# Kernel tuning notes

Hardware: AMD Instinct MI355X
Metric: run time of the kernel (lower is better)

## Reference

```python
import jax, jax.numpy as jnp
import numpy as np
from jax import lax

B, L = 128, 256
DW, DC = 100, 30
H = 400          # hidden_size (bidirectional total)
HD = H // 2      # per-direction hidden
NT = 18          # tag vocab size (BIOES)
VW, VC = 400000, 50000


def setup_inputs():
    key = jax.random.key(0)
    ks = iter(jax.random.split(key, 64))
    rn = lambda shape, s=0.1: jax.random.normal(next(ks), shape, jnp.float32) * s
    inp = {
        "words": jax.random.randint(next(ks), (B, L), 0, VW),
        "cap_words": jax.random.randint(next(ks), (B, L), 0, VC),
        "seq_len": jax.random.randint(next(ks), (B,), L // 2, L + 1),
        "target": jax.random.randint(next(ks), (B, L), 0, NT),
        "word_emb": rn((VW, DW)),
        "char_emb": rn((VC, DC)),
    }
    for l, din in ((0, DW + DC), (1, H)):
        for d in ("f", "b"):
            inp[f"W_ih_l{l}{d}"] = rn((4 * HD, din))
            inp[f"W_hh_l{l}{d}"] = rn((4 * HD, HD))
            inp[f"b_ih_l{l}{d}"] = rn((4 * HD,))
            inp[f"b_hh_l{l}{d}"] = rn((4 * HD,))
    inp["Wf"], inp["bf"] = rn((NT, HD)), jnp.zeros((NT,), jnp.float32)
    inp["Wb"], inp["bb"] = rn((NT, HD)), jnp.zeros((NT,), jnp.float32)
    inp["trans"] = rn((NT, NT))
    return inp


def _lstm_dir(x, W_ih, W_hh, b_ih, b_hh):
    # x: [B, L, D] -> hidden states [B, L, HD]; torch gate order i, f, g, o
    Bsz = x.shape[0]
    def step(carry, xt):
        h, c = carry
        g = xt @ W_ih.T + b_ih + h @ W_hh.T + b_hh
        i, f, gg, o = jnp.split(g, 4, axis=-1)
        c = jax.nn.sigmoid(f) * c + jax.nn.sigmoid(i) * jnp.tanh(gg)
        h = jax.nn.sigmoid(o) * jnp.tanh(c)
        return (h, c), h
    init = (jnp.zeros((Bsz, HD), x.dtype), jnp.zeros((Bsz, HD), x.dtype))
    _, hs = lax.scan(step, init, jnp.swapaxes(x, 0, 1))
    return jnp.swapaxes(hs, 0, 1)


def _rev(x, seq_len):
    # reverse each sequence within its true length (padding stays in place),
    # emulating pack_padded_sequence semantics for the backward direction
    t = jnp.arange(x.shape[1])[None, :]
    idx = jnp.where(t < seq_len[:, None], seq_len[:, None] - 1 - t, t)
    return jnp.take_along_axis(x, idx[:, :, None], axis=1)


def _crf_nll(logits, tags, mask, trans):
    # normalizer: forward algorithm, logsumexp scan over time with mask
    def step(alpha, inp):
        emit, m = inp  # emit: [B, NT], m: [B] bool
        new = jax.nn.logsumexp(alpha[:, :, None] + trans[None] + emit[:, None, :], axis=1)
        return jnp.where(m[:, None], new, alpha), None
    emits = jnp.swapaxes(logits, 0, 1)  # [L, B, NT]
    ms = jnp.swapaxes(mask, 0, 1)
    alpha, _ = lax.scan(step, emits[0], (emits[1:], ms[1:]))
    z = jax.nn.logsumexp(alpha, axis=1)
    # gold path score
    mf = mask.astype(logits.dtype)
    emit_sc = jnp.take_along_axis(logits, tags[:, :, None], axis=2)[:, :, 0]
    gold = jnp.sum(emit_sc * mf, axis=1) + jnp.sum(trans[tags[:, :-1], tags[:, 1:]] * mf[:, 1:], axis=1)
    return z - gold  # per-sample negative log-likelihood, shape [B]


def _model(words, cap_words, seq_len, target, word_emb, char_emb,
           W_ih_l0f, W_hh_l0f, b_ih_l0f, b_hh_l0f, W_ih_l0b, W_hh_l0b, b_ih_l0b, b_hh_l0b,
           W_ih_l1f, W_hh_l1f, b_ih_l1f, b_hh_l1f, W_ih_l1b, W_hh_l1b, b_ih_l1b, b_hh_l1b,
           Wf, bf, Wb, bb, trans):
    mask = jnp.arange(L)[None, :] < seq_len[:, None]  # [B, L] bool
    mf = mask.astype(jnp.float32)[:, :, None]
    x = jnp.concatenate([word_emb[words], char_emb[cap_words]], axis=-1)
    layers = (((W_ih_l0f, W_hh_l0f, b_ih_l0f, b_hh_l0f), (W_ih_l0b, W_hh_l0b, b_ih_l0b, b_hh_l0b)),
              ((W_ih_l1f, W_hh_l1f, b_ih_l1f, b_hh_l1f), (W_ih_l1b, W_hh_l1b, b_ih_l1b, b_hh_l1b)))
    h = x
    for fp, bp in layers:
        fwd = _lstm_dir(h, *fp)
        bwd = _rev(_lstm_dir(_rev(h, seq_len), *bp), seq_len)
        h = jnp.concatenate([fwd, bwd], axis=-1) * mf  # zero padded steps like packed LSTM
    forwards, backwards = h[..., :HD], h[..., HD:]
    logits = forwards @ Wf.T + bf + backwards @ Wb.T + bb
    return _crf_nll(logits, target, mask, trans)


def reference(words, cap_words, seq_len, target, word_emb, char_emb,
              W_ih_l0f, W_hh_l0f, b_ih_l0f, b_hh_l0f, W_ih_l0b, W_hh_l0b, b_ih_l0b, b_hh_l0b,
              W_ih_l1f, W_hh_l1f, b_ih_l1f, b_hh_l1f, W_ih_l1b, W_hh_l1b, b_ih_l1b, b_hh_l1b,
              Wf, bf, Wb, bb, trans):
    return _model(words, cap_words, seq_len, target, word_emb, char_emb,
                  W_ih_l0f, W_hh_l0f, b_ih_l0f, b_hh_l0f, W_ih_l0b, W_hh_l0b, b_ih_l0b, b_hh_l0b,
                  W_ih_l1f, W_hh_l1f, b_ih_l1f, b_hh_l1f, W_ih_l1b, W_hh_l1b, b_ih_l1b, b_hh_l1b,
                  Wf, bf, Wb, bb, trans)
```

## Files before the change

### kernel.cpp

```cpp
#include <hip/hip_runtime.h>
#include <math.h>

#define B_   128
#define L_   256
#define DW_  100
#define DC_  30
#define HD_  200
#define NT_  18
#define SG   4
#define KP0  160
#define KP1  416

typedef _Float16 half8 __attribute__((ext_vector_type(8)));
typedef _Float16 half4 __attribute__((ext_vector_type(4)));
typedef float    f32x4 __attribute__((ext_vector_type(4)));

__device__ __forceinline__ float frcp_(float x) { return __builtin_amdgcn_rcpf(x); }
__device__ __forceinline__ float sigm_(float x) { return frcp_(1.0f + __expf(-x)); }
__device__ __forceinline__ float tanh_(float x) { return 1.0f - 2.0f * frcp_(1.0f + __expf(2.0f * x)); }

__device__ __forceinline__ void barrier_lgkm() {
    asm volatile("s_waitcnt lgkmcnt(0)" ::: "memory");
    __builtin_amdgcn_s_barrier();
    asm volatile("" ::: "memory");
}

__global__ void k_embed(const int* __restrict__ words, const int* __restrict__ caps,
                        const float* __restrict__ wemb, const float* __restrict__ cemb,
                        _Float16* __restrict__ x) {
    int pos = blockIdx.x;
    int w = words[pos], c = caps[pos];
    _Float16* xp = x + (size_t)pos * KP0;
    for (int t = threadIdx.x; t < KP0; t += blockDim.x) {
        float v = 0.f;
        if (t < DW_) v = wemb[(size_t)w * DW_ + t];
        else if (t < DW_ + DC_) v = cemb[(size_t)c * DC_ + (t - DW_)];
        xp[t] = (_Float16)v;
    }
}

__global__ void k_perm_ih16(const float* __restrict__ src, _Float16* __restrict__ dst,
                            int K, int Kpad, int colOff) {
    int i = blockIdx.x * blockDim.x + threadIdx.x;
    if (i >= 800 * Kpad) return;
    int r = i / Kpad, k = i - r * Kpad;
    int jh = r % 200, g = r / 200;
    int col = colOff + (jh << 2) + g;
    dst[(size_t)col * Kpad + k] = (k < K) ? (_Float16)src[(size_t)r * K + k] : (_Float16)0.f;
}

__global__ void k_bias_perm(const float* bi_f, const float* bh_f,
                            const float* bi_b, const float* bh_b, float* bias) {
    int j = blockIdx.x * blockDim.x + threadIdx.x;
    if (j >= 1600) return;
    int dir = j / 800, r = j - dir * 800;
    int col = dir * 800 + ((r % 200) << 2) + (r / 200);
    bias[col] = dir ? (bi_b[r] + bh_b[r]) : (bi_f[r] + bh_f[r]);
}

__global__ void k_wlog(const float* __restrict__ Wf, const float* __restrict__ bfv,
                       const float* __restrict__ Wb, const float* __restrict__ bbv,
                       float* __restrict__ wlog, float* __restrict__ blog) {
    int i = blockIdx.x * blockDim.x + threadIdx.x;
    if (i < NT_ * 400) {
        int t = i / 400, k = i - t * 400;
        wlog[i] = (k < HD_) ? Wf[t * HD_ + k] : Wb[t * HD_ + (k - HD_)];
    }
    if (i < NT_) blog[i] = bfv[i] + bbv[i];
}

__global__ __launch_bounds__(256) void k_gemm16(const _Float16* __restrict__ A,
                                                const _Float16* __restrict__ Bt,
                                                const float* __restrict__ bias,
                                                _Float16* __restrict__ C,
                                                int Kpad) {
    __shared__ __align__(16) _Float16 sA[128 * 40];
    __shared__ __align__(16) _Float16 sB[64 * 40];
    const int tid = threadIdx.x;
    const int w = tid >> 6, l = tid & 63, l15 = l & 15, lq = l >> 4;
    const int m0 = blockIdx.y * 128, n0 = blockIdx.x * 64;
    const int rw = (w >> 1) * 64, cw = (w & 1) * 32;
    f32x4 acc[4][2];
    #pragma unroll
    for (int i = 0; i < 4; i++)
        #pragma unroll
        for (int j = 0; j < 2; j++) acc[i][j] = f32x4{0.f, 0.f, 0.f, 0.f};

    for (int k0 = 0; k0 < Kpad; k0 += 32) {
        {
            int m = tid >> 1, c = (tid & 1) << 4;
            const _Float16* ap = A + (size_t)(m0 + m) * Kpad + k0 + c;
            *(half8*)&sA[m * 40 + c]     = *(const half8*)ap;
            *(half8*)&sA[m * 40 + c + 8] = *(const half8*)(ap + 8);
        }
        {
            int n = tid >> 2, k8 = (tid & 3) << 3;
            *(half8*)&sB[n * 40 + k8] = *(const half8*)&Bt[(size_t)(n0 + n) * Kpad + k0 + k8];
        }
        __syncthreads();
        half8 aF[4], bF[2];
        #pragma unroll
        for (int i = 0; i < 4; i++) aF[i] = *(const half8*)&sA[(rw + i * 16 + l15) * 40 + lq * 8];
        #pragma unroll
        for (int j = 0; j < 2; j++) bF[j] = *(const half8*)&sB[(cw + j * 16 + l15) * 40 + lq * 8];
        #pragma unroll
        for (int i = 0; i < 4; i++)
            #pragma unroll
            for (int j = 0; j < 2; j++)
                acc[i][j] = __builtin_amdgcn_mfma_f32_16x16x32_f16(aF[i], bF[j], acc[i][j], 0, 0, 0);
        __syncthreads();
    }
    #pragma unroll
    for (int j = 0; j < 2; j++) {
        int n = n0 + cw + j * 16 + l15;
        float bv = bias[n];
        #pragma unroll
        for (int i = 0; i < 4; i++) {
            int mrow = m0 + rw + i * 16 + lq * 4;
            #pragma unroll
            for (int r = 0; r < 4; r++)
                C[(size_t)(mrow + r) * 1600 + n] = (_Float16)(acc[i][j][r] + bv);
        }
    }
}

__global__ __launch_bounds__(512, 2) void k_scan7(const _Float16* __restrict__ gates,
                                                  const float* __restrict__ Whh_f,
                                                  const float* __restrict__ Whh_b,
                                                  const int* __restrict__ seq_len,
                                                  _Float16* __restrict__ hout, int ldH) {
    const int dir = blockIdx.x & 1;
    const int b0  = (blockIdx.x >> 1) * SG;
    const int tid = threadIdx.x;
    const int w   = tid >> 6;
    const int l   = tid & 63;
    const int l15 = l & 15;
    const int lq  = l >> 4;

    __shared__ __align__(16) _Float16 hA[2][16 * 232];
    __shared__ __align__(16) _Float16 bEx[2 * 7 * 512];
    __shared__ __align__(16) float    gD[8 * 448];
    __shared__ int ssl[SG];

    const float* W = dir ? Whh_b : Whh_f;
    const int nT = (w < 2) ? 7 : 6;
    const int nCell = nT * 16;

    half8 Breg[6][7];
    #pragma unroll
    for (int i = 0; i < 6; i++) {
        int n  = (w * 6 + i) * 16 + l15;
        int jh = n >> 2, g = n & 3;
        const float* Wr = W + (size_t)(g * 200 + jh) * 200;
        #pragma unroll
        for (int kt = 0; kt < 7; kt++) {
            int k0 = kt * 32 + lq * 8;
            half8 f;
            #pragma unroll
            for (int j = 0; j < 8; j++) {
                int k = k0 + j;
                f[j] = (k < 200) ? (_Float16)Wr[k] : (_Float16)0.f;
            }
            Breg[i][kt] = f;
        }
    }
    if (w < 2) {
        int n  = (48 + w) * 16 + l15;
        int jh = n >> 2, g = n & 3;
        const float* Wr = W + (size_t)(g * 200 + jh) * 200;
        for (int kt = 0; kt < 7; kt++) {
            int k0 = kt * 32 + lq * 8;
            half8 f;
            for (int j = 0; j < 8; j++) {
                int k = k0 + j;
                f[j] = (k < 200) ? (_Float16)Wr[k] : (_Float16)0.f;
            }
            *(half8*)&bEx[(w * 7 + kt) * 512 + l * 8] = f;
        }
    }
    for (int i = tid; i < 2 * 16 * 232; i += 512) (&hA[0][0])[i] = (_Float16)0.f;
    if (tid < SG) ssl[tid] = seq_len[b0 + tid];

    const int  v    = tid;
    const bool stv  = v < 400;
    const int  m_st = v / 100;
    const int  u_st = v - m_st * 100;

    const int cA = l;
    const int iA = cA >> 4, qA = (cA >> 2) & 3, mA = cA & 3;
    const int tgA = (iA < 6) ? (w * 6 + iA) : (48 + w);
    const int hcA = tgA * 4 + qA;
    const int cB = l + 64;
    const int iB = cB >> 4, qB = (cB >> 2) & 3, mB = cB & 3;
    const bool vB = cB < nCell;
    const int tgB = (iB < 6) ? (w * 6 + iB) : (48 + w);
    const int hcB = tgB * 4 + qB;
    float csA = 0.f, csB = 0.f;

    __syncthreads();

    const int slA = ssl[mA];
    const int slB = ssl[mB];
    const int slb_st = stv ? ssl[m_st] : 0;
    const _Float16* gA_base = gates + ((size_t)(b0 + mA) * L_) * 1600 + dir * 800 + 4 * hcA;
    const _Float16* gB_base = gates + ((size_t)(b0 + mB) * L_) * 1600 + dir * 800 + 4 * hcB;
    _Float16* hout_base = hout + (size_t)(b0 + m_st) * L_ * ldH + dir * HD_ + 2 * u_st;

    auto rowOf = [&](int t, int sl) -> int {
        return dir ? ((t < sl) ? sl - 1 - t : t) : t;
    };

    half4 gA0, gA1, gB0, gB1;
    gA0 = *(const half4*)(gA_base + (size_t)rowOf(0, slA) * 1600);
    gA1 = *(const half4*)(gA_base + (size_t)rowOf(1, slA) * 1600);
    if (vB) {
        gB0 = *(const half4*)(gB_base + (size_t)rowOf(0, slB) * 1600);
        gB1 = *(const half4*)(gB_base + (size_t)rowOf(1, slB) * 1600);
    }

    const f32x4 Cz = {0.f, 0.f, 0.f, 0.f};
    for (int t = 0; t < L_; t++) {
        const int p = t & 1;

        if (t > 0 && stv) {
            int tp = t - 1;
            int row = dir ? ((tp < slb_st) ? slb_st - 1 - tp : tp) : tp;
            unsigned int val = (tp < slb_st) ? *(const unsigned int*)&hA[p][m_st * 232 + 2 * u_st] : 0u;
            *(unsigned int*)(hout_base + (size_t)row * ldH) = val;
        }

        f32x4 C[7];
        #pragma unroll
        for (int i = 0; i < 7; i++) C[i] = Cz;
        #pragma unroll
        for (int kt = 0; kt < 7; kt++) {
            half8 hF = *(const half8*)&hA[p][l15 * 232 + kt * 32 + lq * 8];
            #pragma unroll
            for (int i = 0; i < 6; i++)
                C[i] = __builtin_amdgcn_mfma_f32_16x16x32_f16(Breg[i][kt], hF, C[i], 0, 0, 0);
            if (w < 2) {
                half8 bF = *(const half8*)&bEx[(w * 7 + kt) * 512 + l * 8];
                C[6] = __builtin_amdgcn_mfma_f32_16x16x32_f16(bF, hF, C[6], 0, 0, 0);
            }
        }

        if (l15 < 4) {
            #pragma unroll
            for (int i = 0; i < 6; i++)
                *(f32x4*)&gD[w * 448 + (i * 16 + lq * 4 + l15) * 4] = C[i];
            if (w < 2)
                *(f32x4*)&gD[w * 448 + (6 * 16 + lq * 4 + l15) * 4] = C[6];
        }

        {
            f32x4 gv = *(const f32x4*)&gD[w * 448 + cA * 4];
            float xi = gv[0] + (float)gA0[0];
            float xf = gv[1] + (float)gA0[1];
            float xg = gv[2] + (float)gA0[2];
            float xo = gv[3] + (float)gA0[3];
            float cn = sigm_(xf) * csA + sigm_(xi) * tanh_(xg);
            csA = cn;
            hA[1 - p][mA * 232 + hcA] = (_Float16)(sigm_(xo) * tanh_(cn));
        }
        if (vB) {
            f32x4 gv = *(const f32x4*)&gD[w * 448 + cB * 4];
            float xi = gv[0] + (float)gB0[0];
            float xf = gv[1] + (float)gB0[1];
            float xg = gv[2] + (float)gB0[2];
            float xo = gv[3] + (float)gB0[3];
            float cn = sigm_(xf) * csB + sigm_(xi) * tanh_(xg);
            csB = cn;
            hA[1 - p][mB * 232 + hcB] = (_Float16)(sigm_(xo) * tanh_(cn));
        }

        gA0 = gA1;
        gB0 = gB1;
        if (t + 2 < L_) {
            gA1 = *(const half4*)(gA_base + (size_t)rowOf(t + 2, slA) * 1600);
            if (vB) gB1 = *(const half4*)(gB_base + (size_t)rowOf(t + 2, slB) * 1600);
        }

        barrier_lgkm();
    }
    if (stv) {
        int tp = L_ - 1;
        int row = dir ? ((tp < slb_st) ? slb_st - 1 - tp : tp) : tp;
        unsigned int val = (tp < slb_st) ? *(const unsigned int*)&hA[0][m_st * 232 + 2 * u_st] : 0u;
        *(unsigned int*)(hout_base + (size_t)row * ldH) = val;
    }
}

__global__ __launch_bounds__(256) void k_logits(const _Float16* __restrict__ h1,
                                                const float* __restrict__ wlog,
                                                const float* __restrict__ blog,
                                                float* __restrict__ logits) {
    __shared__ float sh[8][400];
    __shared__ float sw[NT_ * 400];
    int p0 = blockIdx.x * 8;
    for (int i = threadIdx.x; i < 8 * 400; i += 256)
        sh[i / 400][i % 400] = (float)h1[(size_t)p0 * 400 + i];
    for (int i = threadIdx.x; i < NT_ * 400; i += 256) sw[i] = wlog[i];
    __syncthreads();
    if (threadIdx.x < 8 * NT_) {
        int pi = threadIdx.x / NT_, tg = threadIdx.x % NT_;
        float a = blog[tg];
        #pragma unroll 4
        for (int k = 0; k < 400; k++) a += sh[pi][k] * sw[tg * 400 + k];
        logits[((size_t)(p0 + pi)) * NT_ + tg] = a;
    }
}

__global__ __launch_bounds__(64) void k_crf(const float* __restrict__ logits,
                                            const int* __restrict__ target,
                                            const int* __restrict__ seq_len,
                                            const float* __restrict__ trans,
                                            float* __restrict__ out) {
    int b = blockIdx.x, tid = threadIdx.x;
    __shared__ float str[NT_ * NT_];
    __shared__ float alpha[NT_];
    __shared__ float sgold[1];
    for (int i = tid; i < NT_ * NT_; i += 64) str[i] = trans[i];
    int sl = seq_len[b];
    const float* lg = logits + (size_t)b * L_ * NT_;
    const int* tg = target + (size_t)b * L_;
    if (tid < NT_) alpha[tid] = lg[tid];
    float gacc = 0.f;
    for (int t = tid; t < L_; t += 64) {
        if (t < sl) {
            gacc += lg[t * NT_ + tg[t]];
            if (t >= 1) gacc += trans[tg[t - 1] * NT_ + tg[t]];
        }
    }
    #pragma unroll
    for (int off = 32; off; off >>= 1) gacc += __shfl_down(gacc, off);
    if (tid == 0) sgold[0] = gacc;
    __syncthreads();
    for (int t = 1; t < L_; t++) {
        if (t < sl) {
            float vv = 0.f;
            if (tid < NT_) {
                float mx = -1e30f;
                #pragma unroll
                for (int i = 0; i < NT_; i++) mx = fmaxf(mx, alpha[i] + str[i * NT_ + tid]);
                float s = 0.f;
                #pragma unroll
                for (int i = 0; i < NT_; i++) s += __expf(alpha[i] + str[i * NT_ + tid] - mx);
                vv = mx + __logf(s) + lg[t * NT_ + tid];
            }
            __syncthreads();
            if (tid < NT_) alpha[tid] = vv;
            __syncthreads();
        }
    }
    if (tid == 0) {
        float mx = -1e30f;
        for (int i = 0; i < NT_; i++) mx = fmaxf(mx, alpha[i]);
        float s = 0.f;
        for (int i = 0; i < NT_; i++) s += __expf(alpha[i] - mx);
        out[b] = (mx + __logf(s)) - sgold[0];
    }
}

extern "C" void kernel_launch(void* const* d_in, const int* in_sizes, int n_in,
                              void* d_out, int out_size, void* d_ws, size_t ws_size,
                              hipStream_t stream) {
    const int*   words  = (const int*)d_in[0];
    const int*   caps   = (const int*)d_in[1];
    const int*   seq    = (const int*)d_in[2];
    const int*   target = (const int*)d_in[3];
    const float* wemb   = (const float*)d_in[4];
    const float* cemb   = (const float*)d_in[5];
    const float* Wih0f  = (const float*)d_in[6];
    const float* Whh0f  = (const float*)d_in[7];
    const float* bih0f  = (const float*)d_in[8];
    const float* bhh0f  = (const float*)d_in[9];
    const float* Wih0b  = (const float*)d_in[10];
    const float* Whh0b  = (const float*)d_in[11];
    const float* bih0b  = (const float*)d_in[12];
    const float* bhh0b  = (const float*)d_in[13];
    const float* Wih1f  = (const float*)d_in[14];
    const float* Whh1f  = (const float*)d_in[15];
    const float* bih1f  = (const float*)d_in[16];
    const float* bhh1f  = (const float*)d_in[17];
    const float* Wih1b  = (const float*)d_in[18];
    const float* Whh1b  = (const float*)d_in[19];
    const float* bih1b  = (const float*)d_in[20];
    const float* bhh1b  = (const float*)d_in[21];
    const float* Wf     = (const float*)d_in[22];
    const float* bfv    = (const float*)d_in[23];
    const float* Wb     = (const float*)d_in[24];
    const float* bbv    = (const float*)d_in[25];
    const float* trans  = (const float*)d_in[26];

    char* base = (char*)d_ws;
    _Float16* gatesH = (_Float16*)(base + 0);
    _Float16* xbuf   = (_Float16*)(base + 104857600);
    _Float16* h0b    = (_Float16*)(base + 115343360);
    _Float16* h1b    = xbuf;
    float* logitsb   = (float*)(base + 142606336);
    _Float16* wihT0  = (_Float16*)(base + 144965632);
    _Float16* wihT1  = (_Float16*)(base + 145477632);
    float* bias0     = (float*)(base + 146808832);
    float* bias1     = (float*)(base + 146815232);
    float* wlog      = (float*)(base + 146821632);
    float* blog      = (float*)(base + 146850432);

    k_perm_ih16<<<(800 * KP0 + 255) / 256, 256, 0, stream>>>(Wih0f, wihT0, 130, KP0, 0);
    k_perm_ih16<<<(800 * KP0 + 255) / 256, 256, 0, stream>>>(Wih0b, wihT0, 130, KP0, 800);
    k_perm_ih16<<<(800 * KP1 + 255) / 256, 256, 0, stream>>>(Wih1f, wihT1, 400, KP1, 0);
    k_perm_ih16<<<(800 * KP1 + 255) / 256, 256, 0, stream>>>(Wih1b, wihT1, 400, KP1, 800);
    k_bias_perm<<<7, 256, 0, stream>>>(bih0f, bhh0f, bih0b, bhh0b, bias0);
    k_bias_perm<<<7, 256, 0, stream>>>(bih1f, bhh1f, bih1b, bhh1b, bias1);
    k_wlog<<<(NT_ * 400 + 255) / 256, 256, 0, stream>>>(Wf, bfv, Wb, bbv, wlog, blog);

    k_embed<<<B_ * L_, 128, 0, stream>>>(words, caps, wemb, cemb, xbuf);

    hipMemsetAsync(h0b, 0, (size_t)32768 * KP1 * sizeof(_Float16), stream);

    k_gemm16<<<dim3(25, 256), 256, 0, stream>>>(xbuf, wihT0, bias0, gatesH, KP0);
    k_scan7<<<(B_ / SG) * 2, 512, 0, stream>>>(gatesH, Whh0f, Whh0b, seq, h0b, KP1);

    k_gemm16<<<dim3(25, 256), 256, 0, stream>>>(h0b, wihT1, bias1, gatesH, KP1);
    k_scan7<<<(B_ / SG) * 2, 512, 0, stream>>>(gatesH, Whh1f, Whh1b, seq, h1b, 400);

    k_logits<<<(B_ * L_) / 8, 256, 0, stream>>>(h1b, wlog, blog, logitsb);
    k_crf<<<B_, 64, 0, stream>>>(logitsb, target, seq, trans, (float*)d_out);
}
```

Before: 1.478 ms.

## Sort batch by sequence length and stop LSTM scan at group max length

A new kernel computes a permutation that sorts batch rows by seq_len, and the scan kernel groups sorted sequences four per block, so each block only iterates up to the longest sequence in its group instead of always running all L steps. Padded positions past the group max are written as zeros after the loop. This removes recurrent timesteps that contribute only padding. It adds a tiny sort kernel and leaves blocks with unequal amounts of work, so total time is set by the longest groups.

```diff
diff --git a/kernel.cpp b/kernel.cpp
--- a/kernel.cpp
+++ b/kernel.cpp
@@ -23,6 +23,20 @@
     asm volatile("s_waitcnt lgkmcnt(0)" ::: "memory");
     __builtin_amdgcn_s_barrier();
     asm volatile("" ::: "memory");
+}
+
+__global__ __launch_bounds__(128) void k_sortperm(const int* __restrict__ seq_len,
+                                                  int* __restrict__ perm) {
+    __shared__ int s[B_];
+    int i = threadIdx.x;
+    s[i] = seq_len[i];
+    __syncthreads();
+    int key = s[i], r = 0;
+    for (int j = 0; j < B_; j++) {
+        int v = s[j];
+        r += (v < key) || (v == key && j < i);
+    }
+    perm[r] = i;
 }
 
 __global__ void k_embed(const int* __restrict__ words, const int* __restrict__ caps,
@@ -124,10 +138,11 @@
     }
 }
 
-__global__ __launch_bounds__(512, 2) void k_scan7(const _Float16* __restrict__ gates,
+__global__ __launch_bounds__(512, 2) void k_scan9(const _Float16* __restrict__ gates,
                                                   const float* __restrict__ Whh_f,
                                                   const float* __restrict__ Whh_b,
                                                   const int* __restrict__ seq_len,
+                                                  const int* __restrict__ perm,
                                                   _Float16* __restrict__ hout, int ldH) {
     const int dir = blockIdx.x & 1;
     const int b0  = (blockIdx.x >> 1) * SG;
@@ -141,6 +156,7 @@
     __shared__ __align__(16) _Float16 bEx[2 * 7 * 512];
     __shared__ __align__(16) float    gD[8 * 448];
     __shared__ int ssl[SG];
+    __shared__ int spb[SG];
 
     const float* W = dir ? Whh_b : Whh_f;
     const int nT = (w < 2) ? 7 : 6;
@@ -179,7 +195,11 @@
         }
     }
     for (int i = tid; i < 2 * 16 * 232; i += 512) (&hA[0][0])[i] = (_Float16)0.f;
-    if (tid < SG) ssl[tid] = seq_len[b0 + tid];
+    if (tid < SG) {
+        int ob = perm[b0 + tid];
+        spb[tid] = ob;
+        ssl[tid] = seq_len[ob];
+    }
 
     const int  v    = tid;
     const bool stv  = v < 400;
@@ -199,12 +219,15 @@
 
     __syncthreads();
 
+    const int slmax = max(max(ssl[0], ssl[1]), max(ssl[2], ssl[3]));
+
     const int slA = ssl[mA];
     const int slB = ssl[mB];
     const int slb_st = stv ? ssl[m_st] : 0;
-    const _Float16* gA_base = gates + ((size_t)(b0 + mA) * L_) * 1600 + dir * 800 + 4 * hcA;
-    const _Float16* gB_base = gates + ((size_t)(b0 + mB) * L_) * 1600 + dir * 800 + 4 * hcB;
-    _Float16* hout_base = hout + (size_t)(b0 + m_st) * L_ * ldH + dir * HD_ + 2 * u_st;
+    const _Float16* gA_base = gates + ((size_t)spb[mA] * L_) * 1600 + dir * 800 + 4 * hcA;
+    const _Float16* gB_base = gates + ((size_t)spb[mB] * L_) * 1600 + dir * 800 + 4 * hcB;
+    _Float16* hout_base = stv ? (hout + (size_t)spb[m_st] * L_ * ldH + dir * HD_ + 2 * u_st)
+                              : hout;
 
     auto rowOf = [&](int t, int sl) -> int {
         return dir ? ((t < sl) ? sl - 1 - t : t) : t;
@@ -219,7 +242,7 @@
     }
 
     const f32x4 Cz = {0.f, 0.f, 0.f, 0.f};
-    for (int t = 0; t < L_; t++) {
+    for (int t = 0; t < slmax; t++) {
         const int p = t & 1;
 
         if (t > 0 && stv) {
@@ -283,10 +306,14 @@
         barrier_lgkm();
     }
     if (stv) {
-        int tp = L_ - 1;
+        int tp = slmax - 1;
         int row = dir ? ((tp < slb_st) ? slb_st - 1 - tp : tp) : tp;
-        unsigned int val = (tp < slb_st) ? *(const unsigned int*)&hA[0][m_st * 232 + 2 * u_st] : 0u;
+        unsigned int val = (tp < slb_st) ? *(const unsigned int*)&hA[slmax & 1][m_st * 232 + 2 * u_st] : 0u;
         *(unsigned int*)(hout_base + (size_t)row * ldH) = val;
+    }
+    if (stv) {
+        for (int tp = slmax; tp < L_; tp++)
+            *(unsigned int*)(hout_base + (size_t)tp * ldH) = 0u;
     }
 }
 
@@ -404,6 +431,7 @@
     float* bias1     = (float*)(base + 146815232);
     float* wlog      = (float*)(base + 146821632);
     float* blog      = (float*)(base + 146850432);
+    int*   permb     = (int*)(base + 146850560);
 
     k_perm_ih16<<<(800 * KP0 + 255) / 256, 256, 0, stream>>>(Wih0f, wihT0, 130, KP0, 0);
     k_perm_ih16<<<(800 * KP0 + 255) / 256, 256, 0, stream>>>(Wih0b, wihT0, 130, KP0, 800);
@@ -412,16 +440,17 @@
     k_bias_perm<<<7, 256, 0, stream>>>(bih0f, bhh0f, bih0b, bhh0b, bias0);
     k_bias_perm<<<7, 256, 0, stream>>>(bih1f, bhh1f, bih1b, bhh1b, bias1);
     k_wlog<<<(NT_ * 400 + 255) / 256, 256, 0, stream>>>(Wf, bfv, Wb, bbv, wlog, blog);
+    k_sortperm<<<1, 128, 0, stream>>>(seq, permb);
 
     k_embed<<<B_ * L_, 128, 0, stream>>>(words, caps, wemb, cemb, xbuf);
 
     hipMemsetAsync(h0b, 0, (size_t)32768 * KP1 * sizeof(_Float16), stream);
 
     k_gemm16<<<dim3(25, 256), 256, 0, stream>>>(xbuf, wihT0, bias0, gatesH, KP0);
-    k_scan7<<<(B_ / SG) * 2, 512, 0, stream>>>(gatesH, Whh0f, Whh0b, seq, h0b, KP1);
+    k_scan9<<<(B_ / SG) * 2, 512, 0, stream>>>(gatesH, Whh0f, Whh0b, seq, permb, h0b, KP1);
 
     k_gemm16<<<dim3(25, 256), 256, 0, stream>>>(h0b, wihT1, bias1, gatesH, KP1);
-    k_scan7<<<(B_ / SG) * 2, 512, 0, stream>>>(gatesH, Whh1f, Whh1b, seq, h1b, 400);
+    k_scan9<<<(B_ / SG) * 2, 512, 0, stream>>>(gatesH, Whh1f, Whh1b, seq, permb, h1b, 400);
 
     k_logits<<<(B_ * L_) / 8, 256, 0, stream>>>(h1b, wlog, blog, logitsb);
     k_crf<<<B_, 64, 0, stream>>>(logitsb, target, seq, trans, (float*)d_out);
```

Result: no change. 1.468 ms (-0.7%).
